# Performance work log

Measured on AMD Instinct MI355X. Metric: run time of the kernel, lower is better.

Reference implementation:

```python
import jax, jax.numpy as jnp
import numpy as np

K = 3          # kernel size
K2 = K * K     # ope_channels


def setup_inputs() -> dict:
    key = jax.random.key(0)
    k1, k2, k3, k4, k5 = jax.random.split(key, 5)
    b, c, h, w = 8, 64, 128, 128
    out_c = 64
    x = jax.random.normal(k1, (b, c, h, w), dtype=jnp.float32)
    # conv weight: (in_channels, out_channels, k, k) as in the torch module
    weight = jax.random.normal(k2, (c, out_c, K, K), dtype=jnp.float32) * 0.05
    bias = jax.random.normal(k3, (out_c,), dtype=jnp.float32) * 0.05
    # operator MLP: Linear(K2 -> K2*K2); torch weight layout (out_features, in_features)
    op_w = jax.random.normal(k4, (K2 * K2, K2), dtype=jnp.float32) * 0.1
    op_b = jax.random.normal(k5, (K2 * K2,), dtype=jnp.float32) * 0.01
    return {"x": x, "weight": weight, "bias": bias, "op_w": op_w, "op_b": op_b}


def _unfold(x):
    # F.unfold(kernel=3, stride=1, pad=1) -> patches ordered (c, ki, kj)
    b, c, h, w = x.shape
    xp = jnp.pad(x, ((0, 0), (0, 0), (1, 1), (1, 1)))
    # (b, c, K2, h, w) with K2 ordered row-major over (ki, kj), matching torch
    patches = jnp.stack([xp[:, :, i:i + h, j:j + w]
                         for i in range(K) for j in range(K)], axis=2)
    return patches.transpose(0, 1, 3, 4, 2)  # (b, c, h, w, K2)


def reference(x, weight, bias, op_w, op_b):
    b, c, h, w = x.shape
    xu = _unfold(x)  # (b, c, h, w, K2)
    # per-pixel patch norm over channels -> (b, h, w, K2)
    n = jnp.sqrt(jnp.sum(xu * xu, axis=1))
    # per-pixel dynamic operator: (b, h, w, K2, K2)
    op = jnp.tanh(n @ op_w.T + op_b).reshape(b, h, w, K2, K2)
    # apply operator: bchw j , bhw jk -> bchw k
    x_op = jnp.einsum('bchwj,bhwjk->bchwk', xu, op)
    # final conv weight contraction: weight (in, out, K, K) -> (out, in, K2)
    wr = weight.reshape(c, -1, K2).transpose(1, 0, 2)
    out = jnp.einsum('bchwk,ock->bohw', x_op + xu, wr)
    return out + bias[None, :, None, None]
```

## Files before the change

### kernel.cpp

```cpp
#include <hip/hip_runtime.h>
#include <math.h>
#include <stdint.h>

#define HW   128
#define CIN  64
#define OC   64
#define TW   16
#define TH   4
#define HLW  18
#define HLH  6
#define HLN  (HLW*HLH)
#define SXR  109
#define K2   9
#define KTOT (CIN*K2)
#define SOPW 54

typedef __bf16  bf16x8 __attribute__((ext_vector_type(8)));
typedef float   f32x4  __attribute__((ext_vector_type(4)));
typedef uint32_t u32x4 __attribute__((ext_vector_type(4)));

__device__ __forceinline__ ushort f32_to_bf16_rne(float f) {
    union { float f; uint32_t u; } x; x.f = f;
    return (ushort)((x.u + 0x7FFF + ((x.u >> 16) & 1)) >> 16);
}
__device__ __forceinline__ float bflo(uint32_t w) { return __uint_as_float(w << 16); }
__device__ __forceinline__ float bfhi(uint32_t w) { return __uint_as_float(w & 0xffff0000u); }

#define PKBF16(dst, lo, hi) \
    asm("v_cvt_pk_bf16_f32 %0, %1, %2" : "=v"(dst) : "v"(lo), "v"(hi))

__global__ void prep_weight(const float* __restrict__ w, ushort* __restrict__ wt) {
    int n = blockIdx.x * 256 + threadIdx.x;
    int o = n / KTOT;
    int r = n - o * KTOT;
    int kt = r >> 6;
    int c  = r & 63;
    wt[n] = f32_to_bf16_rne(w[(c * OC + o) * K2 + kt]);
}

__global__ __launch_bounds__(256, 3)
void dyf_main(const float* __restrict__ x,
              const float* __restrict__ bias,
              const float* __restrict__ op_w,
              const float* __restrict__ op_b,
              const ushort* __restrict__ wt,
              float* __restrict__ out)
{
    __shared__ float    sx[CIN * SXR];
    __shared__ float    sT[HLN];
    __shared__ uint32_t sopp[64 * SOPW];

    const int tid  = threadIdx.x;
    const int lane = tid & 63;
    const int wv   = tid >> 6;
    const int b    = blockIdx.z;
    const int h0   = blockIdx.y * TH;
    const int w0   = blockIdx.x * TW;

    {
        const float* __restrict__ xb = x + (size_t)b * CIN * HW * HW;
        #pragma unroll
        for (int it = 0; it < 27; ++it) {
            int i  = tid + it * 256;
            int c  = i / HLN;
            int r  = i - c * HLN;
            int hy = r / HLW;
            int hx = r - hy * HLW;
            int gy = h0 - 1 + hy;
            int gx = w0 - 1 + hx;
            float v = 0.f;
            if ((unsigned)gy < HW && (unsigned)gx < HW)
                v = xb[c * HW * HW + gy * HW + gx];
            sx[c * SXR + r] = v;
        }
    }
    __syncthreads();

    if (tid < HLN) {
        float s = 0.f;
        #pragma unroll 16
        for (int c = 0; c < CIN; ++c) { float v = sx[c * SXR + tid]; s += v * v; }
        sT[tid] = s;
    }
    __syncthreads();

    {
        const int px = tid >> 2;
        const int q  = tid & 3;
        const int py = px >> 4, pxx = px & 15;
        float nrm[9];
        #pragma unroll
        for (int j = 0; j < 9; ++j)
            nrm[j] = sqrtf(sT[(py + j / 3) * HLW + pxx + (j % 3)]);
        const int nkt = (q == 0) ? 3 : 2;
        for (int t = 0; t < 3; ++t) {
            if (t >= nkt) break;
            const int kt = (q == 0) ? ((t == 2) ? 8 : t) : (q * 2 + t);
            float tv[9];
            #pragma unroll
            for (int j = 0; j < 9; ++j) {
                const int m = j * 9 + kt;
                float a = op_b[m];
                #pragma unroll
                for (int jj = 0; jj < 9; ++jj) a += nrm[jj] * op_w[m * 9 + jj];
                tv[j] = tanhf(a);
            }
            tv[kt] += 1.0f;
            const float fz = 0.0f;
            uint32_t pw0, pw1, pw2, pw3, pw4;
            PKBF16(pw0, tv[0], tv[1]);
            PKBF16(pw1, tv[2], tv[3]);
            PKBF16(pw2, tv[4], tv[5]);
            PKBF16(pw3, tv[6], tv[7]);
            PKBF16(pw4, tv[8], fz);
            uint32_t* d = &sopp[px * SOPW + kt * 6];
            d[0] = pw0; d[1] = pw1; d[2] = pw2; d[3] = pw3; d[4] = pw4;
        }
    }
    __syncthreads();

    const int pxx = lane & 15;
    const int g   = lane >> 4;
    const int py  = wv;

    uint32_t ow[45];
    {
        const uint32_t* srcp = &sopp[(wv * 16 + pxx) * SOPW];
        #pragma unroll
        for (int kt = 0; kt < 9; ++kt) {
            uint2 a = *reinterpret_cast<const uint2*>(srcp + kt * 6);
            uint2 c = *reinterpret_cast<const uint2*>(srcp + kt * 6 + 2);
            ow[kt * 5 + 0] = a.x; ow[kt * 5 + 1] = a.y;
            ow[kt * 5 + 2] = c.x; ow[kt * 5 + 3] = c.y;
            ow[kt * 5 + 4] = srcp[kt * 6 + 4];
        }
    }

    f32x4 acc[4];
    #pragma unroll
    for (int mr = 0; mr < 4; ++mr) acc[mr] = f32x4{0.f, 0.f, 0.f, 0.f};

    #pragma unroll
    for (int chalf = 0; chalf < 2; ++chalf) {
        u32x4 zh[9];
        #pragma unroll
        for (int t = 0; t < 4; ++t) {
            const int c0 = chalf * 32 + g * 8 + 2 * t;
            float xu0[9], xu1[9];
            #pragma unroll
            for (int j = 0; j < 9; ++j) {
                const int pos = (py + j / 3) * HLW + pxx + (j % 3);
                xu0[j] = sx[c0 * SXR + pos];
                xu1[j] = sx[(c0 + 1) * SXR + pos];
            }
            #pragma unroll
            for (int kt = 0; kt < 9; ++kt) {
                float opv[9];
                opv[0] = bflo(ow[kt*5+0]); opv[1] = bfhi(ow[kt*5+0]);
                opv[2] = bflo(ow[kt*5+1]); opv[3] = bfhi(ow[kt*5+1]);
                opv[4] = bflo(ow[kt*5+2]); opv[5] = bfhi(ow[kt*5+2]);
                opv[6] = bflo(ow[kt*5+3]); opv[7] = bfhi(ow[kt*5+3]);
                opv[8] = bflo(ow[kt*5+4]);
                float y0 = 0.f, y1 = 0.f;
                #pragma unroll
                for (int j = 0; j < 9; ++j) {
                    y0 += xu0[j] * opv[j];
                    y1 += xu1[j] * opv[j];
                }
                uint32_t pk;
                PKBF16(pk, y0, y1);
                zh[kt][t] = pk;
            }
        }
        #pragma unroll
        for (int kt = 0; kt < 9; ++kt) {
            const int s = 2 * kt + chalf;
            const bf16x8 bfr = __builtin_bit_cast(bf16x8, zh[kt]);
            #pragma unroll
            for (int mr = 0; mr < 4; ++mr) {
                const bf16x8 af = *reinterpret_cast<const bf16x8*>(
                    wt + (mr * 16 + pxx) * KTOT + s * 32 + g * 8);
                acc[mr] = __builtin_amdgcn_mfma_f32_16x16x32_bf16(af, bfr, acc[mr], 0, 0, 0);
            }
        }
    }

    #pragma unroll
    for (int mr = 0; mr < 4; ++mr) {
        #pragma unroll
        for (int ii = 0; ii < 4; ++ii) {
            const int o = mr * 16 + g * 4 + ii;
            out[(((size_t)b * OC + o) * HW + (h0 + wv)) * HW + w0 + pxx]
                = acc[mr][ii] + bias[o];
        }
    }
}

extern "C" void kernel_launch(void* const* d_in, const int* in_sizes, int n_in,
                              void* d_out, int out_size, void* d_ws, size_t ws_size,
                              hipStream_t stream) {
    const float* x      = (const float*)d_in[0];
    const float* weight = (const float*)d_in[1];
    const float* bias   = (const float*)d_in[2];
    const float* op_w   = (const float*)d_in[3];
    const float* op_b   = (const float*)d_in[4];
    float*  out = (float*)d_out;
    ushort* wt  = (ushort*)d_ws;

    prep_weight<<<dim3((OC * KTOT) / 256), dim3(256), 0, stream>>>(weight, wt);

    dim3 grid(HW / TW, HW / TH, 8);
    dyf_main<<<grid, dim3(256), 0, stream>>>(x, bias, op_w, op_b, wt, out);
}
```

Before: 236.5 us.

## Reorder operator apply loop to cut register pressure and pin occupancy

The loop order in the operator-apply stage is inverted: all 8 channels' 3x3 patches are loaded first, then for each of the 9 kernel taps the per-pixel operator row is read from shared memory and fed straight into the MFMA. This removes the 45-register operator cache and the 9 staged B fragments (zh), which should cut VGPR pressure so the kernel can hold 3 waves per EU, now requested via amdgpu_waves_per_eu. The cost is repeated LDS reads of the operator row per channel half and 72 live patch floats.

```diff
diff --git a/kernel.cpp b/kernel.cpp
--- a/kernel.cpp
+++ b/kernel.cpp
@@ -38,7 +38,8 @@
     wt[n] = f32_to_bf16_rne(w[(c * OC + o) * K2 + kt]);
 }
 
-__global__ __launch_bounds__(256, 3)
+__global__ __launch_bounds__(256)
+__attribute__((amdgpu_waves_per_eu(3, 3)))
 void dyf_main(const float* __restrict__ x,
               const float* __restrict__ bias,
               const float* __restrict__ op_w,
@@ -122,19 +123,7 @@
     const int pxx = lane & 15;
     const int g   = lane >> 4;
     const int py  = wv;
-
-    uint32_t ow[45];
-    {
-        const uint32_t* srcp = &sopp[(wv * 16 + pxx) * SOPW];
-        #pragma unroll
-        for (int kt = 0; kt < 9; ++kt) {
-            uint2 a = *reinterpret_cast<const uint2*>(srcp + kt * 6);
-            uint2 c = *reinterpret_cast<const uint2*>(srcp + kt * 6 + 2);
-            ow[kt * 5 + 0] = a.x; ow[kt * 5 + 1] = a.y;
-            ow[kt * 5 + 2] = c.x; ow[kt * 5 + 3] = c.y;
-            ow[kt * 5 + 4] = srcp[kt * 6 + 4];
-        }
-    }
+    const uint32_t* __restrict__ oprow = &sopp[(wv * 16 + pxx) * SOPW];
 
     f32x4 acc[4];
     #pragma unroll
@@ -142,40 +131,49 @@
 
     #pragma unroll
     for (int chalf = 0; chalf < 2; ++chalf) {
-        u32x4 zh[9];
-        #pragma unroll
-        for (int t = 0; t < 4; ++t) {
-            const int c0 = chalf * 32 + g * 8 + 2 * t;
-            float xu0[9], xu1[9];
+        float xu[8][9];
+        #pragma unroll
+        for (int cc = 0; cc < 8; ++cc) {
+            const int c = chalf * 32 + g * 8 + cc;
             #pragma unroll
-            for (int j = 0; j < 9; ++j) {
-                const int pos = (py + j / 3) * HLW + pxx + (j % 3);
-                xu0[j] = sx[c0 * SXR + pos];
-                xu1[j] = sx[(c0 + 1) * SXR + pos];
-            }
-            #pragma unroll
-            for (int kt = 0; kt < 9; ++kt) {
-                float opv[9];
-                opv[0] = bflo(ow[kt*5+0]); opv[1] = bfhi(ow[kt*5+0]);
-                opv[2] = bflo(ow[kt*5+1]); opv[3] = bfhi(ow[kt*5+1]);
-                opv[4] = bflo(ow[kt*5+2]); opv[5] = bfhi(ow[kt*5+2]);
-                opv[6] = bflo(ow[kt*5+3]); opv[7] = bfhi(ow[kt*5+3]);
-                opv[8] = bflo(ow[kt*5+4]);
-                float y0 = 0.f, y1 = 0.f;
+            for (int r = 0; r < 3; ++r) {
+                const int pos = c * SXR + (py + r) * HLW + pxx;
+                xu[cc][3 * r + 0] = sx[pos];
+                xu[cc][3 * r + 1] = sx[pos + 1];
+                xu[cc][3 * r + 2] = sx[pos + 2];
+            }
+        }
+        #pragma unroll
+        for (int kt = 0; kt < 9; ++kt) {
+            const uint2 a  = *reinterpret_cast<const uint2*>(oprow + kt * 6);
+            const uint2 cw = *reinterpret_cast<const uint2*>(oprow + kt * 6 + 2);
+            const uint32_t e = oprow[kt * 6 + 4];
+            float opv[9];
+            opv[0] = bflo(a.x);  opv[1] = bfhi(a.x);
+            opv[2] = bflo(a.y);  opv[3] = bfhi(a.y);
+            opv[4] = bflo(cw.x); opv[5] = bfhi(cw.x);
+            opv[6] = bflo(cw.y); opv[7] = bfhi(cw.y);
+            opv[8] = bflo(e);
+
+            uint32_t pk0, pk1, pk2, pk3;
+            {
+                float y0 = 0.f, y1 = 0.f, y2 = 0.f, y3 = 0.f;
+                float y4 = 0.f, y5 = 0.f, y6 = 0.f, y7 = 0.f;
                 #pragma unroll
                 for (int j = 0; j < 9; ++j) {
-                    y0 += xu0[j] * opv[j];
-                    y1 += xu1[j] * opv[j];
+                    y0 += xu[0][j] * opv[j];  y1 += xu[1][j] * opv[j];
+                    y2 += xu[2][j] * opv[j];  y3 += xu[3][j] * opv[j];
+                    y4 += xu[4][j] * opv[j];  y5 += xu[5][j] * opv[j];
+                    y6 += xu[6][j] * opv[j];  y7 += xu[7][j] * opv[j];
                 }
-                uint32_t pk;
-                PKBF16(pk, y0, y1);
-                zh[kt][t] = pk;
-            }
-        }
-        #pragma unroll
-        for (int kt = 0; kt < 9; ++kt) {
+                PKBF16(pk0, y0, y1);
+                PKBF16(pk1, y2, y3);
+                PKBF16(pk2, y4, y5);
+                PKBF16(pk3, y6, y7);
+            }
+            u32x4 fr; fr[0] = pk0; fr[1] = pk1; fr[2] = pk2; fr[3] = pk3;
+            const bf16x8 bfr = __builtin_bit_cast(bf16x8, fr);
             const int s = 2 * kt + chalf;
-            const bf16x8 bfr = __builtin_bit_cast(bf16x8, zh[kt]);
             #pragma unroll
             for (int mr = 0; mr < 4; ++mr) {
                 const bf16x8 af = *reinterpret_cast<const bf16x8*>(
```

Result: slower. 255.2 us (+7.9%).
